# Optimization experiments

Measured on AMD Instinct MI355X. Metric: run time of the kernel, lower is better.

The kernel has to match this reference:

```python
import jax, jax.numpy as jnp
import numpy as np
import math

# init kwargs (constants)
HSHIFT, VSHIFT, ANGLE = 2, 2, 2
BS, C, H, W = 2048, 1, 64, 64


def setup_inputs() -> dict:
    key = jax.random.key(0)
    k1, k2 = jax.random.split(key)
    fm1 = jax.random.normal(k1, (BS, C, H, W), dtype=jnp.float32)
    fm2 = jax.random.normal(k2, (BS, C, H, W), dtype=jnp.float32)
    return {"fm1": fm1, "fm2": fm2}


def _warp_rotate(img, theta_deg, h, w):
    """Equivalent of cv2.warpAffine(img, cv2.getRotationMatrix2D((w/2,h/2), theta, 1)).

    img: [bs, h, w]. Bilinear interpolation, constant-0 border.
    Returns (rotated_img [bs,h,w], rotated_ones_mask [h,w]).
    cv2 inverts the forward map internally; inverse of rotation by theta about
    the center is rotation by -theta about the center.
    """
    t = -theta_deg * (math.pi / 180.0)
    alpha = jnp.cos(t)
    beta = jnp.sin(t)
    cx, cy = w / 2.0, h / 2.0
    ys, xs = jnp.meshgrid(jnp.arange(h, dtype=jnp.float32),
                          jnp.arange(w, dtype=jnp.float32), indexing="ij")
    x_src = alpha * xs + beta * ys + (1.0 - alpha) * cx - beta * cy
    y_src = -beta * xs + alpha * ys + beta * cx + (1.0 - alpha) * cy

    x0 = jnp.floor(x_src)
    y0 = jnp.floor(y_src)
    wx = x_src - x0
    wy = y_src - y0
    x0i = x0.astype(jnp.int32)
    y0i = y0.astype(jnp.int32)

    out = jnp.zeros_like(img)
    msk = jnp.zeros((h, w), img.dtype)
    corners = ((0, 0, (1 - wy) * (1 - wx)), (0, 1, (1 - wy) * wx),
               (1, 0, wy * (1 - wx)), (1, 1, wy * wx))
    for dy, dx, wgt in corners:
        yi = y0i + dy
        xi = x0i + dx
        valid = ((yi >= 0) & (yi < h) & (xi >= 0) & (xi < w)).astype(img.dtype)
        yc = jnp.clip(yi, 0, h - 1)
        xc = jnp.clip(xi, 0, w - 1)
        out = out + (wgt * valid) * img[:, yc, xc]
        msk = msk + wgt * valid
    return out, msk


def _forward(fm1, fm2):
    bs, c, h, w = fm1.shape
    thetas = jnp.arange(-ANGLE, ANGLE + 1, dtype=jnp.float32)
    min_dist = jnp.full((bs,), jnp.finfo(jnp.float32).max, dtype=jnp.float32)
    for bh in range(-HSHIFT, HSHIFT + 1):
        for bv in range(-VSHIFT, VSHIFT + 1):
            if bh >= 0:
                r1, r2 = fm1[:, :, :, :w - bh], fm2[:, :, :, bh:]
            else:
                r1, r2 = fm1[:, :, :, -bh:], fm2[:, :, :, :w + bh]
            if bv >= 0:
                r1, r2 = r1[:, :, :h - bv, :], r2[:, :, bv:, :]
            else:
                r1, r2 = r1[:, :, -bv:, :], r2[:, :, :h + bv, :]
            oh, ow = r1.shape[2], r1.shape[3]
            r1s = r1[:, 0]  # [bs, oh, ow] (C==1)
            # original detaches ref2 before warping (cv2 path)
            r2s = jax.lax.stop_gradient(r2[:, 0])

            def one_theta(theta, r1s=r1s, r2s=r2s, oh=oh, ow=ow):
                rr2, mk = _warp_rotate(r2s, theta, oh, ow)
                se = ((r1s - rr2) ** 2) * mk  # [bs, oh, ow]
                return se.reshape(se.shape[0], -1).sum(1) / mk.sum()

            dists = jax.vmap(one_theta)(thetas)  # [ntheta, bs]
            min_dist = jnp.minimum(min_dist, dists.min(0))
    return min_dist


def reference(fm1, fm2):
    return _forward(fm1, fm2)
```

## Files before the change

### kernel.cpp

```cpp
#include <hip/hip_runtime.h>
#include <hip/hip_fp16.h>
#include <math.h>

#define NTH 5
#define GLO 66
#define GHI 132
#define PS (GLO + 4096 + GHI)

#define ALP0 0.99939082701909576f
#define ALP1 0.99984769515639127f
constexpr float ALPc[5] = {ALP0, ALP1, 1.0f, ALP1, ALP0};
constexpr float BETc[5] = {0.03489949670250097f, 0.01745240643728351f, 0.0f,
                           -0.01745240643728351f, -0.03489949670250097f};

__device__ __forceinline__ unsigned h2bits(float a, float b) {
    __half2 h = __floats2half2_rn(a, b);
    return *(unsigned*)&h;
}
__device__ __forceinline__ __half2 h2(unsigned u) { return *(__half2*)&u; }

__device__ __forceinline__ int pkadd(int a, int b) {
    __half2 r = __hadd2(*(__half2*)&a, *(__half2*)&b);
    return *(int*)&r;
}
__device__ __forceinline__ int hred16(__half2 v) {
    int x = *(int*)&v;
    int t = __builtin_amdgcn_update_dpp(0, x, 0xB1, 0xF, 0xF, true);
    x = pkadd(x, t);
    t = __builtin_amdgcn_update_dpp(0, x, 0x4E, 0xF, 0xF, true);
    x = pkadd(x, t);
    t = __builtin_amdgcn_update_dpp(0, x, 0x141, 0xF, 0xF, true);
    x = pkadd(x, t);
    t = __builtin_amdgcn_update_dpp(0, x, 0x140, 0xF, 0xF, true);
    x = pkadd(x, t);
    return x;
}

__global__ void pack_kernel(const float* __restrict__ fm1,
                            const float* __restrict__ fm2,
                            __half* __restrict__ fm1h,
                            __half* __restrict__ fm2h) {
    const int g = blockIdx.x;
    const int tid = threadIdx.x;
    const size_t inb = (size_t)g * 16 * 4096;
    for (int p = tid; p < 4096; p += 1024) {
        uint4 wa, wb, va, vb;
        wa.x = h2bits(fm1[inb + 0 * 4096 + p], fm1[inb + 1 * 4096 + p]);
        wa.y = h2bits(fm1[inb + 2 * 4096 + p], fm1[inb + 3 * 4096 + p]);
        wa.z = h2bits(fm1[inb + 4 * 4096 + p], fm1[inb + 5 * 4096 + p]);
        wa.w = h2bits(fm1[inb + 6 * 4096 + p], fm1[inb + 7 * 4096 + p]);
        wb.x = h2bits(fm1[inb + 8 * 4096 + p], fm1[inb + 9 * 4096 + p]);
        wb.y = h2bits(fm1[inb + 10 * 4096 + p], fm1[inb + 11 * 4096 + p]);
        wb.z = h2bits(fm1[inb + 12 * 4096 + p], fm1[inb + 13 * 4096 + p]);
        wb.w = h2bits(fm1[inb + 14 * 4096 + p], fm1[inb + 15 * 4096 + p]);
        va.x = h2bits(fm2[inb + 0 * 4096 + p], fm2[inb + 1 * 4096 + p]);
        va.y = h2bits(fm2[inb + 2 * 4096 + p], fm2[inb + 3 * 4096 + p]);
        va.z = h2bits(fm2[inb + 4 * 4096 + p], fm2[inb + 5 * 4096 + p]);
        va.w = h2bits(fm2[inb + 6 * 4096 + p], fm2[inb + 7 * 4096 + p]);
        vb.x = h2bits(fm2[inb + 8 * 4096 + p], fm2[inb + 9 * 4096 + p]);
        vb.y = h2bits(fm2[inb + 10 * 4096 + p], fm2[inb + 11 * 4096 + p]);
        vb.z = h2bits(fm2[inb + 12 * 4096 + p], fm2[inb + 13 * 4096 + p]);
        vb.w = h2bits(fm2[inb + 14 * 4096 + p], fm2[inb + 15 * 4096 + p]);
        uint4* d1 = (uint4*)(fm1h + ((size_t)g * 4096 + p) * 16);
        d1[0] = wa;
        d1[1] = wb;
        *(uint4*)(fm2h + ((size_t)(g * 2 + 0) * 4096 + p) * 8) = va;
        *(uint4*)(fm2h + ((size_t)(g * 2 + 1) * 4096 + p) * 8) = vb;
    }
}

__global__ void table_kernel(uint4* __restrict__ tab) {
    const int bid = blockIdx.x;
    const int s = bid >> 2, tj = bid & 3;
    const int ti = tj < 2 ? tj : tj + 1;
    const int tid = threadIdx.x;
    const int bh = (s / 5) - 2;
    const int bv = (s % 5) - 2;
    const int ox2 = bh >= 0 ? bh : 0;
    const int ow = 64 - (bh >= 0 ? bh : -bh);
    const int oy2 = bv >= 0 ? bv : 0;
    const int oh = 64 - (bv >= 0 ? bv : -bv);
    const float cx = 0.5f * (float)ow;
    const float cy = 0.5f * (float)oh;
    const float alpha = ALPc[ti], beta = BETc[ti];
    for (int i = 0; i < 16; i++) {
        const int px = tid + 256 * i;
        const int y = px >> 6, x = px & 63;
        uint4 e = make_uint4(0u, 0u, 0u, (unsigned)GLO);
        if (x < ow && y < oh) {
            const float xs = (float)x, yf = (float)y;
            const float hx = fmaf(alpha, xs, (1.0f - alpha) * cx - beta * cy);
            const float hy = fmaf(-beta, xs, beta * cx + (1.0f - alpha) * cy);
            const float xsrc = fmaf(beta, yf, hx);
            const float ysrc = fmaf(alpha, yf, hy);
            const float x0f = floorf(xsrc), y0f = floorf(ysrc);
            const float wx = xsrc - x0f, wy = ysrc - y0f;
            const int x0 = (int)x0f, y0 = (int)y0f;
            const float ax0 = ((unsigned)x0 < (unsigned)ow) ? (1.f - wx) : 0.f;
            const float ax1 = ((unsigned)(x0 + 1) < (unsigned)ow) ? wx : 0.f;
            const float ay0 = ((unsigned)y0 < (unsigned)oh) ? (1.f - wy) : 0.f;
            const float ay1 = ((unsigned)(y0 + 1) < (unsigned)oh) ? wy : 0.f;
            const int x0c = min(max(x0, -1), ow - 1);
            const int y0c = min(max(y0, -1), oh - 1);
            const float mk = (ax0 + ax1) * (ay0 + ay1);
            e.x = h2bits(ay0 * ax0, ay0 * ax1);
            e.y = h2bits(ay1 * ax0, ay1 * ax1);
            e.z = h2bits(mk, 0.0f);
            e.w = (unsigned)(GLO + (y0c + oy2) * 64 + (x0c + ox2));
        }
        tab[(size_t)bid * 4096 + px] = e;
    }
}

__global__ void denom_kernel(float* __restrict__ denom) {
    const int bid = blockIdx.x;
    const int s = bid / 5, ti = bid % 5;
    const int lane = threadIdx.x;
    const int bh = (s / 5) - 2;
    const int bv = (s % 5) - 2;
    const int ow = 64 - (bh >= 0 ? bh : -bh);
    const int oh = 64 - (bv >= 0 ? bv : -bv);
    const float cx = 0.5f * (float)ow;
    const float cy = 0.5f * (float)oh;
    const float alpha = ALPc[ti], beta = BETc[ti];
    float acc = 0.0f;
    if (lane < ow) {
        const float xs = (float)lane;
        const float hx = fmaf(alpha, xs, (1.0f - alpha) * cx - beta * cy);
        const float hy = fmaf(-beta, xs, beta * cx + (1.0f - alpha) * cy);
        for (int y = 0; y < oh; y++) {
            const float yf = (float)y;
            const float xsrc = fmaf(beta, yf, hx);
            const float ysrc = fmaf(alpha, yf, hy);
            const float x0f = floorf(xsrc), y0f = floorf(ysrc);
            const float wx = xsrc - x0f, wy = ysrc - y0f;
            const int x0 = (int)x0f, y0 = (int)y0f;
            const float ax0 = ((unsigned)x0 < (unsigned)ow) ? (1.f - wx) : 0.f;
            const float ax1 = ((unsigned)(x0 + 1) < (unsigned)ow) ? wx : 0.f;
            const float ay0 = ((unsigned)y0 < (unsigned)oh) ? (1.f - wy) : 0.f;
            const float ay1 = ((unsigned)(y0 + 1) < (unsigned)oh) ? wy : 0.f;
            acc += (ax0 + ax1) * (ay0 + ay1);
        }
    }
    #pragma unroll
    for (int off = 32; off; off >>= 1) acc += __shfl_xor(acc, off);
    if (lane == 0) denom[bid] = acc;
}

__launch_bounds__(1024, 1)
__global__ void wrsl_main(const __half* __restrict__ fm1h,
                          const __half* __restrict__ fm2h,
                          const uint4* __restrict__ tab,
                          const float* __restrict__ denom,
                          float* __restrict__ out) {
    __shared__ uint4 lds[2 * PS];
    __shared__ float redm[16][4][80];
    __shared__ float colsum[80];

    const int tid = threadIdx.x;
    const int g = blockIdx.x >> 1;
    const int hf = blockIdx.x & 1;
    const int sBeg = hf ? 13 : 0;
    const int sEnd = hf ? 25 : 13;

    {
        const uint4* src = (const uint4*)(fm2h + (size_t)g * 2 * 4096 * 8);
        for (int i = tid; i < 4096; i += 1024) {
            lds[GLO + i] = src[i];
            lds[PS + GLO + i] = src[4096 + i];
        }
        if (tid < 2 * (GLO + GHI)) {
            const int pl = (tid >= GLO + GHI) ? 1 : 0;
            const int j = tid - pl * (GLO + GHI);
            const int off = (j < GLO) ? j : (GLO + 4096 + (j - GLO));
            lds[pl * PS + off] = make_uint4(0u, 0u, 0u, 0u);
        }
    }
    const int lane = tid & 63, wid = tid >> 6;
    __syncthreads();

    float best = 3.4028234663852886e38f;

    for (int s = sBeg; s < sEnd; s++) {
        const int bh = (s / 5) - 2;
        const int bv = (s % 5) - 2;
        const int ox1 = bh >= 0 ? 0 : -bh;
        const int ox2 = bh >= 0 ? bh : 0;
        const int ow = 64 - (bh >= 0 ? bh : -bh);
        const int oy1 = bv >= 0 ? 0 : -bv;
        const int oy2 = bv >= 0 ? bv : 0;
        const int oh = 64 - (bv >= 0 ? bv : -bv);
        const int xcap = ox1 + min(lane, ow - 1);

        uint4 nrA[4], nrB[4];
        #pragma unroll
        for (int k = 0; k < 4; k++) {
            const int p1 = (oy1 + min(wid + 16 * k, oh - 1)) * 64 + xcap;
            const uint4* rp = (const uint4*)(fm1h + ((size_t)g * 4096 + p1) * 16);
            uint4 a = rp[0], b = rp[1];
            a.x ^= 0x80008000u; a.y ^= 0x80008000u; a.z ^= 0x80008000u; a.w ^= 0x80008000u;
            b.x ^= 0x80008000u; b.y ^= 0x80008000u; b.z ^= 0x80008000u; b.w ^= 0x80008000u;
            nrA[k] = a;
            nrB[k] = b;
        }

        #pragma unroll
        for (int tj = 0; tj < 4; tj++) {
            const int ti = tj < 2 ? tj : tj + 1;
            const uint4* tq = tab + (size_t)(s * 4 + tj) * 4096;
            uint4 tv[4];
            #pragma unroll
            for (int k = 0; k < 4; k++)
                tv[k] = tq[(wid + 16 * k) * 64 + lane];

            const __half2 z2 = __float2half2_rn(0.0f);
            __half2 seA[4] = {z2, z2, z2, z2};
            __half2 seB[4] = {z2, z2, z2, z2};
            #pragma unroll
            for (int k = 0; k < 4; k++) {
                const __half2 tx = h2(tv[k].x), ty = h2(tv[k].y);
                const __half2 w00p = __low2half2(tx), w01p = __high2half2(tx);
                const __half2 w10p = __low2half2(ty), w11p = __high2half2(ty);
                const __half2 mkp = __low2half2(h2(tv[k].z));
                const int b0 = (int)tv[k].w;
                {
                    const uint4 q00 = lds[b0], q01 = lds[b0 + 1];
                    const uint4 q10 = lds[b0 + 64], q11 = lds[b0 + 65];
                    #define FULL(SE, NR, C)                                    \
                    {                                                          \
                        __half2 r = __hfma2(w00p, h2(q00.C), h2(NR[k].C));     \
                        r = __hfma2(w01p, h2(q01.C), r);                       \
                        r = __hfma2(w10p, h2(q10.C), r);                       \
                        r = __hfma2(w11p, h2(q11.C), r);                       \
                        SE = __hfma2(__hmul2(r, mkp), r, SE);                  \
                    }
                    FULL(seA[0], nrA, x) FULL(seA[1], nrA, y)
                    FULL(seA[2], nrA, z) FULL(seA[3], nrA, w)
                    #undef FULL
                }
                {
                    const uint4 q00 = lds[PS + b0], q01 = lds[PS + b0 + 1];
                    const uint4 q10 = lds[PS + b0 + 64], q11 = lds[PS + b0 + 65];
                    #define FULL(SE, NR, C)                                    \
                    {                                                          \
                        __half2 r = __hfma2(w00p, h2(q00.C), h2(NR[k].C));     \
                        r = __hfma2(w01p, h2(q01.C), r);                       \
                        r = __hfma2(w10p, h2(q10.C), r);                       \
                        r = __hfma2(w11p, h2(q11.C), r);                       \
                        SE = __hfma2(__hmul2(r, mkp), r, SE);                  \
                    }
                    FULL(seB[0], nrB, x) FULL(seB[1], nrB, y)
                    FULL(seB[2], nrB, z) FULL(seB[3], nrB, w)
                    #undef FULL
                }
            }
            int ra0 = hred16(seA[0]), ra1 = hred16(seA[1]);
            int ra2 = hred16(seA[2]), ra3 = hred16(seA[3]);
            int rb0 = hred16(seB[0]), rb1 = hred16(seB[1]);
            int rb2 = hred16(seB[2]), rb3 = hred16(seB[3]);
            if ((lane & 15) == 0) {
                float2 f0 = __half22float2(h2(ra0)), f1 = __half22float2(h2(ra1));
                float2 f2 = __half22float2(h2(ra2)), f3 = __half22float2(h2(ra3));
                float2 f4 = __half22float2(h2(rb0)), f5 = __half22float2(h2(rb1));
                float2 f6 = __half22float2(h2(rb2)), f7 = __half22float2(h2(rb3));
                float4* dst = (float4*)&redm[wid][lane >> 4][ti * 16];
                dst[0] = make_float4(f0.x, f0.y, f1.x, f1.y);
                dst[1] = make_float4(f2.x, f2.y, f3.x, f3.y);
                dst[2] = make_float4(f4.x, f4.y, f5.x, f5.y);
                dst[3] = make_float4(f6.x, f6.y, f7.x, f7.y);
            }
        }

        {
            const float xinf = (lane < ow) ? 1.0f : 0.0f;
            const __half2 z2 = __float2half2_rn(0.0f);
            __half2 seA[4] = {z2, z2, z2, z2};
            __half2 seB[4] = {z2, z2, z2, z2};
            #pragma unroll
            for (int k = 0; k < 4; k++) {
                const int y = wid + 16 * k;
                const __half2 msk = __float2half2_rn((y < oh) ? xinf : 0.0f);
                const int idx = GLO + (oy2 + y) * 64 + ox2 + lane;
                const uint4 qa = lds[idx];
                const uint4 qb = lds[PS + idx];
                #define LIGHT(SE, NR, Q, C)                                     \
                {                                                               \
                    __half2 d = __hmul2(__hadd2(h2(Q.C), h2(NR[k].C)), msk);    \
                    SE = __hfma2(d, d, SE);                                     \
                }
                LIGHT(seA[0], nrA, qa, x) LIGHT(seA[1], nrA, qa, y)
                LIGHT(seA[2], nrA, qa, z) LIGHT(seA[3], nrA, qa, w)
                LIGHT(seB[0], nrB, qb, x) LIGHT(seB[1], nrB, qb, y)
                LIGHT(seB[2], nrB, qb, z) LIGHT(seB[3], nrB, qb, w)
                #undef LIGHT
            }
            int ra0 = hred16(seA[0]), ra1 = hred16(seA[1]);
            int ra2 = hred16(seA[2]), ra3 = hred16(seA[3]);
            int rb0 = hred16(seB[0]), rb1 = hred16(seB[1]);
            int rb2 = hred16(seB[2]), rb3 = hred16(seB[3]);
            if ((lane & 15) == 0) {
                float2 f0 = __half22float2(h2(ra0)), f1 = __half22float2(h2(ra1));
                float2 f2 = __half22float2(h2(ra2)), f3 = __half22float2(h2(ra3));
                float2 f4 = __half22float2(h2(rb0)), f5 = __half22float2(h2(rb1));
                float2 f6 = __half22float2(h2(rb2)), f7 = __half22float2(h2(rb3));
                float4* dst = (float4*)&redm[wid][lane >> 4][2 * 16];
                dst[0] = make_float4(f0.x, f0.y, f1.x, f1.y);
                dst[1] = make_float4(f2.x, f2.y, f3.x, f3.y);
                dst[2] = make_float4(f4.x, f4.y, f5.x, f5.y);
                dst[3] = make_float4(f6.x, f6.y, f7.x, f7.y);
            }
        }

        __syncthreads();
        if (tid < 80) {
            float sum = 0.0f;
            #pragma unroll 8
            for (int w = 0; w < 16; w++) {
                sum += redm[w][0][tid] + redm[w][1][tid] + redm[w][2][tid] + redm[w][3][tid];
            }
            colsum[tid] = sum;
        }
        __syncthreads();
        if (tid < 16) {
            #pragma unroll
            for (int t2 = 0; t2 < NTH; t2++)
                best = fminf(best, colsum[t2 * 16 + tid] / denom[s * 5 + t2]);
        }
    }
    if (tid < 16)
        atomicMin((unsigned int*)&out[g * 16 + tid], __float_as_uint(best));
}

extern "C" void kernel_launch(void* const* d_in, const int* in_sizes, int n_in,
                              void* d_out, int out_size, void* d_ws, size_t ws_size,
                              hipStream_t stream) {
    const float* fm1 = (const float*)d_in[0];
    const float* fm2 = (const float*)d_in[1];
    float* out = (float*)d_out;
    __half* fm1h = (__half*)d_ws;
    __half* fm2h = (__half*)((char*)d_ws + (16u << 20));
    uint4* tab = (uint4*)((char*)d_ws + (32u << 20));
    float* denom = (float*)((char*)d_ws + (32u << 20) + 100u * 4096u * 16u);

    hipMemsetAsync(d_out, 0x7F, (size_t)out_size * 4, stream);
    pack_kernel<<<128, 1024, 0, stream>>>(fm1, fm2, fm1h, fm2h);
    table_kernel<<<100, 256, 0, stream>>>(tab);
    denom_kernel<<<125, 64, 0, stream>>>(denom);
    wrsl_main<<<256, 1024, 0, stream>>>(fm1h, fm2h, tab, denom, out);
}
```

Before: 218.0 us.

## Split each 16-image group into two 8-image planes across twice as many blocks

Each block of the main kernel now handles one 8-image half-plane instead of a full 16-image group, halving LDS use and per-thread register state, and the grid doubles from 256 to 512 blocks. fm1 packing is changed to the same plane-split layout so each block reads one uint4 per pixel. The launch bound min-blocks hint is raised so more blocks can be resident per CU, which targets better occupancy and latency hiding. In exchange the table reads and per-shift bookkeeping are repeated per plane, adding redundant table traffic and synchronisation.

Result: faster. 205.9 us (-5.6%).

```diff
diff --git a/kernel.cpp b/kernel.cpp
--- a/kernel.cpp
+++ b/kernel.cpp
@@ -61,9 +61,8 @@
         vb.y = h2bits(fm2[inb + 10 * 4096 + p], fm2[inb + 11 * 4096 + p]);
         vb.z = h2bits(fm2[inb + 12 * 4096 + p], fm2[inb + 13 * 4096 + p]);
         vb.w = h2bits(fm2[inb + 14 * 4096 + p], fm2[inb + 15 * 4096 + p]);
-        uint4* d1 = (uint4*)(fm1h + ((size_t)g * 4096 + p) * 16);
-        d1[0] = wa;
-        d1[1] = wb;
+        *(uint4*)(fm1h + ((size_t)(g * 2 + 0) * 4096 + p) * 8) = wa;
+        *(uint4*)(fm1h + ((size_t)(g * 2 + 1) * 4096 + p) * 8) = wb;
         *(uint4*)(fm2h + ((size_t)(g * 2 + 0) * 4096 + p) * 8) = va;
         *(uint4*)(fm2h + ((size_t)(g * 2 + 1) * 4096 + p) * 8) = vb;
     }
@@ -147,33 +146,32 @@
     if (lane == 0) denom[bid] = acc;
 }
 
-__launch_bounds__(1024, 1)
+__launch_bounds__(1024, 8)
 __global__ void wrsl_main(const __half* __restrict__ fm1h,
                           const __half* __restrict__ fm2h,
                           const uint4* __restrict__ tab,
                           const float* __restrict__ denom,
                           float* __restrict__ out) {
-    __shared__ uint4 lds[2 * PS];
-    __shared__ float redm[16][4][80];
-    __shared__ float colsum[80];
+    __shared__ uint4 lds[PS];
+    __shared__ float redm[16][4][40];
+    __shared__ float colsum[40];
 
     const int tid = threadIdx.x;
-    const int g = blockIdx.x >> 1;
+    const int g = blockIdx.x >> 2;
+    const int pl = (blockIdx.x >> 1) & 1;
     const int hf = blockIdx.x & 1;
     const int sBeg = hf ? 13 : 0;
     const int sEnd = hf ? 25 : 13;
+    const size_t pbase = (size_t)(g * 2 + pl) * 4096;
 
     {
-        const uint4* src = (const uint4*)(fm2h + (size_t)g * 2 * 4096 * 8);
-        for (int i = tid; i < 4096; i += 1024) {
-            lds[GLO + i] = src[i];
-            lds[PS + GLO + i] = src[4096 + i];
-        }
-        if (tid < 2 * (GLO + GHI)) {
-            const int pl = (tid >= GLO + GHI) ? 1 : 0;
-            const int j = tid - pl * (GLO + GHI);
-            const int off = (j < GLO) ? j : (GLO + 4096 + (j - GLO));
-            lds[pl * PS + off] = make_uint4(0u, 0u, 0u, 0u);
+        const uint4* src = (const uint4*)(fm2h + pbase * 8);
+        #pragma unroll
+        for (int i = 0; i < 4; i++)
+            lds[GLO + tid + 1024 * i] = src[tid + 1024 * i];
+        if (tid < GLO + GHI) {
+            const int off = (tid < GLO) ? tid : (4096 + tid);
+            lds[off] = make_uint4(0u, 0u, 0u, 0u);
         }
     }
     const int lane = tid & 63, wid = tid >> 6;
@@ -192,16 +190,13 @@
         const int oh = 64 - (bv >= 0 ? bv : -bv);
         const int xcap = ox1 + min(lane, ow - 1);
 
-        uint4 nrA[4], nrB[4];
+        uint4 nr[4];
         #pragma unroll
         for (int k = 0; k < 4; k++) {
             const int p1 = (oy1 + min(wid + 16 * k, oh - 1)) * 64 + xcap;
-            const uint4* rp = (const uint4*)(fm1h + ((size_t)g * 4096 + p1) * 16);
-            uint4 a = rp[0], b = rp[1];
+            uint4 a = *(const uint4*)(fm1h + (pbase + p1) * 8);
             a.x ^= 0x80008000u; a.y ^= 0x80008000u; a.z ^= 0x80008000u; a.w ^= 0x80008000u;
-            b.x ^= 0x80008000u; b.y ^= 0x80008000u; b.z ^= 0x80008000u; b.w ^= 0x80008000u;
-            nrA[k] = a;
-            nrB[k] = b;
+            nr[k] = a;
         }
 
         #pragma unroll
@@ -214,8 +209,7 @@
                 tv[k] = tq[(wid + 16 * k) * 64 + lane];
 
             const __half2 z2 = __float2half2_rn(0.0f);
-            __half2 seA[4] = {z2, z2, z2, z2};
-            __half2 seB[4] = {z2, z2, z2, z2};
+            __half2 se[4] = {z2, z2, z2, z2};
             #pragma unroll
             for (int k = 0; k < 4; k++) {
                 const __half2 tx = h2(tv[k].x), ty = h2(tv[k].y);
@@ -223,96 +217,61 @@
                 const __half2 w10p = __low2half2(ty), w11p = __high2half2(ty);
                 const __half2 mkp = __low2half2(h2(tv[k].z));
                 const int b0 = (int)tv[k].w;
-                {
-                    const uint4 q00 = lds[b0], q01 = lds[b0 + 1];
-                    const uint4 q10 = lds[b0 + 64], q11 = lds[b0 + 65];
-                    #define FULL(SE, NR, C)                                    \
-                    {                                                          \
-                        __half2 r = __hfma2(w00p, h2(q00.C), h2(NR[k].C));     \
-                        r = __hfma2(w01p, h2(q01.C), r);                       \
-                        r = __hfma2(w10p, h2(q10.C), r);                       \
-                        r = __hfma2(w11p, h2(q11.C), r);                       \
-                        SE = __hfma2(__hmul2(r, mkp), r, SE);                  \
-                    }
-                    FULL(seA[0], nrA, x) FULL(seA[1], nrA, y)
-                    FULL(seA[2], nrA, z) FULL(seA[3], nrA, w)
-                    #undef FULL
+                const uint4 q00 = lds[b0], q01 = lds[b0 + 1];
+                const uint4 q10 = lds[b0 + 64], q11 = lds[b0 + 65];
+                #define FULL(SE, C)                                        \
+                {                                                          \
+                    __half2 r = __hfma2(w00p, h2(q00.C), h2(nr[k].C));     \
+                    r = __hfma2(w01p, h2(q01.C), r);                       \
+                    r = __hfma2(w10p, h2(q10.C), r);                       \
+                    r = __hfma2(w11p, h2(q11.C), r);                       \
+                    SE = __hfma2(__hmul2(r, mkp), r, SE);                  \
                 }
-                {
-                    const uint4 q00 = lds[PS + b0], q01 = lds[PS + b0 + 1];
-                    const uint4 q10 = lds[PS + b0 + 64], q11 = lds[PS + b0 + 65];
-                    #define FULL(SE, NR, C)                                    \
-                    {                                                          \
-                        __half2 r = __hfma2(w00p, h2(q00.C), h2(NR[k].C));     \
-                        r = __hfma2(w01p, h2(q01.C), r);                       \
-                        r = __hfma2(w10p, h2(q10.C), r);                       \
-                        r = __hfma2(w11p, h2(q11.C), r);                       \
-                        SE = __hfma2(__hmul2(r, mkp), r, SE);                  \
-                    }
-                    FULL(seB[0], nrB, x) FULL(seB[1], nrB, y)
-                    FULL(seB[2], nrB, z) FULL(seB[3], nrB, w)
-                    #undef FULL
-                }
-            }
-            int ra0 = hred16(seA[0]), ra1 = hred16(seA[1]);
-            int ra2 = hred16(seA[2]), ra3 = hred16(seA[3]);
-            int rb0 = hred16(seB[0]), rb1 = hred16(seB[1]);
-            int rb2 = hred16(seB[2]), rb3 = hred16(seB[3]);
+                FULL(se[0], x) FULL(se[1], y) FULL(se[2], z) FULL(se[3], w)
+                #undef FULL
+            }
+            int r0 = hred16(se[0]), r1 = hred16(se[1]);
+            int r2 = hred16(se[2]), r3 = hred16(se[3]);
             if ((lane & 15) == 0) {
-                float2 f0 = __half22float2(h2(ra0)), f1 = __half22float2(h2(ra1));
-                float2 f2 = __half22float2(h2(ra2)), f3 = __half22float2(h2(ra3));
-                float2 f4 = __half22float2(h2(rb0)), f5 = __half22float2(h2(rb1));
-                float2 f6 = __half22float2(h2(rb2)), f7 = __half22float2(h2(rb3));
-                float4* dst = (float4*)&redm[wid][lane >> 4][ti * 16];
+                float2 f0 = __half22float2(h2(r0)), f1 = __half22float2(h2(r1));
+                float2 f2 = __half22float2(h2(r2)), f3 = __half22float2(h2(r3));
+                float4* dst = (float4*)&redm[wid][lane >> 4][ti * 8];
                 dst[0] = make_float4(f0.x, f0.y, f1.x, f1.y);
                 dst[1] = make_float4(f2.x, f2.y, f3.x, f3.y);
-                dst[2] = make_float4(f4.x, f4.y, f5.x, f5.y);
-                dst[3] = make_float4(f6.x, f6.y, f7.x, f7.y);
             }
         }
 
         {
             const float xinf = (lane < ow) ? 1.0f : 0.0f;
             const __half2 z2 = __float2half2_rn(0.0f);
-            __half2 seA[4] = {z2, z2, z2, z2};
-            __half2 seB[4] = {z2, z2, z2, z2};
+            __half2 se[4] = {z2, z2, z2, z2};
             #pragma unroll
             for (int k = 0; k < 4; k++) {
                 const int y = wid + 16 * k;
                 const __half2 msk = __float2half2_rn((y < oh) ? xinf : 0.0f);
                 const int idx = GLO + (oy2 + y) * 64 + ox2 + lane;
                 const uint4 qa = lds[idx];
-                const uint4 qb = lds[PS + idx];
-                #define LIGHT(SE, NR, Q, C)                                     \
-                {                                                               \
-                    __half2 d = __hmul2(__hadd2(h2(Q.C), h2(NR[k].C)), msk);    \
-                    SE = __hfma2(d, d, SE);                                     \
+                #define LIGHT(SE, C)                                        \
+                {                                                           \
+                    __half2 d = __hmul2(__hadd2(h2(qa.C), h2(nr[k].C)), msk); \
+                    SE = __hfma2(d, d, SE);                                 \
                 }
-                LIGHT(seA[0], nrA, qa, x) LIGHT(seA[1], nrA, qa, y)
-                LIGHT(seA[2], nrA, qa, z) LIGHT(seA[3], nrA, qa, w)
-                LIGHT(seB[0], nrB, qb, x) LIGHT(seB[1], nrB, qb, y)
-                LIGHT(seB[2], nrB, qb, z) LIGHT(seB[3], nrB, qb, w)
+                LIGHT(se[0], x) LIGHT(se[1], y) LIGHT(se[2], z) LIGHT(se[3], w)
                 #undef LIGHT
             }
-            int ra0 = hred16(seA[0]), ra1 = hred16(seA[1]);
-            int ra2 = hred16(seA[2]), ra3 = hred16(seA[3]);
-            int rb0 = hred16(seB[0]), rb1 = hred16(seB[1]);
-            int rb2 = hred16(seB[2]), rb3 = hred16(seB[3]);
+            int r0 = hred16(se[0]), r1 = hred16(se[1]);
+            int r2 = hred16(se[2]), r3 = hred16(se[3]);
             if ((lane & 15) == 0) {
-                float2 f0 = __half22float2(h2(ra0)), f1 = __half22float2(h2(ra1));
-                float2 f2 = __half22float2(h2(ra2)), f3 = __half22float2(h2(ra3));
-                float2 f4 = __half22float2(h2(rb0)), f5 = __half22float2(h2(rb1));
-                float2 f6 = __half22float2(h2(rb2)), f7 = __half22float2(h2(rb3));
-                float4* dst = (float4*)&redm[wid][lane >> 4][2 * 16];
+                float2 f0 = __half22float2(h2(r0)), f1 = __half22float2(h2(r1));
+                float2 f2 = __half22float2(h2(r2)), f3 = __half22float2(h2(r3));
+                float4* dst = (float4*)&redm[wid][lane >> 4][2 * 8];
                 dst[0] = make_float4(f0.x, f0.y, f1.x, f1.y);
                 dst[1] = make_float4(f2.x, f2.y, f3.x, f3.y);
-                dst[2] = make_float4(f4.x, f4.y, f5.x, f5.y);
-                dst[3] = make_float4(f6.x, f6.y, f7.x, f7.y);
             }
         }
 
         __syncthreads();
-        if (tid < 80) {
+        if (tid < 40) {
             float sum = 0.0f;
             #pragma unroll 8
             for (int w = 0; w < 16; w++) {
@@ -321,14 +280,14 @@
             colsum[tid] = sum;
         }
         __syncthreads();
-        if (tid < 16) {
+        if (tid < 8) {
             #pragma unroll
             for (int t2 = 0; t2 < NTH; t2++)
-                best = fminf(best, colsum[t2 * 16 + tid] / denom[s * 5 + t2]);
-        }
-    }
-    if (tid < 16)
-        atomicMin((unsigned int*)&out[g * 16 + tid], __float_as_uint(best));
+                best = fminf(best, colsum[t2 * 8 + tid] / denom[s * 5 + t2]);
+        }
+    }
+    if (tid < 8)
+        atomicMin((unsigned int*)&out[g * 16 + pl * 8 + tid], __float_as_uint(best));
 }
 
 extern "C" void kernel_launch(void* const* d_in, const int* in_sizes, int n_in,
@@ -346,5 +305,5 @@
     pack_kernel<<<128, 1024, 0, stream>>>(fm1, fm2, fm1h, fm2h);
     table_kernel<<<100, 256, 0, stream>>>(tab);
     denom_kernel<<<125, 64, 0, stream>>>(denom);
-    wrsl_main<<<256, 1024, 0, stream>>>(fm1h, fm2h, tab, denom, out);
-}
+    wrsl_main<<<512, 1024, 0, stream>>>(fm1h, fm2h, tab, denom, out);
+}
```
